# Optimization experiments

Hardware: AMD Instinct MI355X
Metric: run time of the kernel (lower is better)

The kernel has to match this reference:

```python
import jax, jax.numpy as jnp
import numpy as np

N = 500000      # gaussians
D = 256         # d_model
H = 8           # heads
DFF = 1024      # ffn hidden
L = 2           # encoder layers
VS = 0.0625     # voxel_size
MR = 10         # multires (both embedders)
EPS = 1e-5      # layernorm eps


def _embed(x, nf):
    freqs = 2.0 ** jnp.arange(nf, dtype=x.dtype)
    xf = x[..., None, :] * freqs[:, None]                  # [..., F, 3]
    sc = jnp.stack([jnp.sin(xf), jnp.cos(xf)], axis=-2)    # [..., F, 2, 3]
    return jnp.concatenate([x, sc.reshape(*x.shape[:-1], nf * 2 * 3)], axis=-1)


def _ln(x, w, b):
    m = x.mean(-1, keepdims=True)
    v = ((x - m) ** 2).mean(-1, keepdims=True)
    return (x - m) / jnp.sqrt(v + EPS) * w + b


def _mha(x, wi, bi, wo, bo):
    U, d = x.shape
    dh = d // H
    qkv = x @ wi.T + bi                                    # [U, 3d]
    q, k, v = jnp.split(qkv, 3, axis=-1)
    sp = lambda t: t.reshape(U, H, dh).transpose(1, 0, 2)  # [H, U, dh]
    q, k, v = sp(q), sp(k), sp(v)
    scale = 1.0 / jnp.sqrt(jnp.asarray(dh, x.dtype))
    attn = jax.nn.softmax(jnp.einsum('hqd,hkd->hqk', q, k) * scale, axis=-1)
    o = jnp.einsum('hqk,hkd->hqd', attn, v).transpose(1, 0, 2).reshape(U, d)
    return o @ wo.T + bo


def setup_inputs() -> dict:
    key = jax.random.key(0)
    ks = jax.random.split(key, 24)
    centres = jax.random.uniform(ks[0], (N, 3), dtype=jnp.float32)
    feats = jax.random.normal(ks[1], (N, D), dtype=jnp.float32)
    # voxelize + unique (data-dependent -> precompute, round() has zero grad anyway)
    vp = np.round(np.asarray(centres) / VS) * VS
    _, inv = np.unique(vp, axis=0, return_inverse=True)
    inv = inv.reshape(-1)
    U = int(inv.max()) + 1
    s = 0.02
    rn = lambda k, shp: jax.random.normal(k, shp, dtype=jnp.float32) * s
    PE = MR * 2 * 3 + 3  # 63
    return dict(
        gaussian_centres=centres,
        gaussian_features=feats,
        inverse_indices=jnp.asarray(inv, jnp.int32),
        num_unique=U,
        in_proj_w=rn(ks[2], (L, 3 * D, D)), in_proj_b=rn(ks[3], (L, 3 * D)),
        out_proj_w=rn(ks[4], (L, D, D)), out_proj_b=rn(ks[5], (L, D)),
        lin1_w=rn(ks[6], (L, DFF, D)), lin1_b=rn(ks[7], (L, DFF)),
        lin2_w=rn(ks[8], (L, D, DFF)), lin2_b=rn(ks[9], (L, D)),
        norm1_w=jnp.ones((L, D), jnp.float32), norm1_b=jnp.zeros((L, D), jnp.float32),
        norm2_w=jnp.ones((L, D), jnp.float32), norm2_b=jnp.zeros((L, D), jnp.float32),
        pe_w1=rn(ks[10], (D, PE)), pe_b1=rn(ks[11], (D,)),
        pe_w2=rn(ks[12], (D, D)), pe_b2=rn(ks[13], (D,)),
        dm_w1=rn(ks[14], (D, D + PE)), dm_b1=rn(ks[15], (D,)),
        dm_w2=rn(ks[16], (D, D)), dm_b2=rn(ks[17], (D,)),
    )


def reference(gaussian_centres, gaussian_features, inverse_indices, num_unique,
              in_proj_w, in_proj_b, out_proj_w, out_proj_b,
              lin1_w, lin1_b, lin2_w, lin2_b,
              norm1_w, norm1_b, norm2_w, norm2_b,
              pe_w1, pe_b1, pe_w2, pe_b2,
              dm_w1, dm_b1, dm_w2, dm_b2):
    # 1-4: voxelize + segment-sum features per unique voxel
    vp = jnp.round(gaussian_centres / VS) * VS
    agg = jax.ops.segment_sum(gaussian_features, inverse_indices, num_segments=num_unique)  # [U, D]
    uv = jnp.zeros((num_unique, 3), gaussian_centres.dtype).at[inverse_indices].set(vp)     # unique voxel coords
    # learnable positional encoding MLP
    pe = _embed(uv, MR)
    pe = jax.nn.leaky_relu(pe @ pe_w1.T + pe_b1, 0.01) @ pe_w2.T + pe_b2
    # transformer encoder (post-LN, relu, eval mode -> no dropout)
    x = agg + pe
    for l in range(L):
        x = _ln(x + _mha(x, in_proj_w[l], in_proj_b[l], out_proj_w[l], out_proj_b[l]),
                norm1_w[l], norm1_b[l])
        ff = jax.nn.relu(x @ lin1_w[l].T + lin1_b[l]) @ lin2_w[l].T + lin2_b[l]
        x = _ln(x + ff, norm2_w[l], norm2_b[l])
    # 6-7: gather back to per-gaussian rows
    rec = x[inverse_indices]                                # [N, D]
    # delta MLP: cat([pos_encoding, features])
    d_in = jnp.concatenate([_embed(gaussian_centres, MR), rec], axis=-1)
    delta = jax.nn.leaky_relu(d_in @ dm_w1.T + dm_b1, 0.01) @ dm_w2.T + dm_b2
    return rec + delta
```

## Files before the change

### kernel.cpp

```cpp
#include <hip/hip_runtime.h>
#include <math.h>

#define NG   500000
#define DM   256
#define NH   8
#define DHD  32
#define DFF  1024
#define NLAY 2
#define PED  63
#define VSF  0.0625f
#define EPSF 1e-5f
#define UP   4928
#define MAXU 4913
#define NQT  77
#define NDBLK 7813
#define SCL  0.17677669529663687f

typedef short bf16x8 __attribute__((ext_vector_type(8)));
typedef float f32x4 __attribute__((ext_vector_type(4)));

__device__ __forceinline__ float lrelu(float v){ return v >= 0.f ? v : 0.01f*v; }

__device__ __forceinline__ short f2b(float f){
  unsigned u = __float_as_uint(f);
  return (short)((u + 0x7fffu + ((u >> 16) & 1u)) >> 16);
}

__device__ __forceinline__ f32x4 mfma16(bf16x8 a, bf16x8 b, f32x4 c){
  return __builtin_amdgcn_mfma_f32_16x16x32_bf16(a, b, c, 0, 0, 0);
}

__device__ __forceinline__ float embed_elem(float cx, float cy, float cz, int j){
  if (j == 0) return cx;
  if (j == 1) return cy;
  if (j == 2) return cz;
  int q = j - 3;
  int f = q / 6;
  int r = q - f*6;
  int c = r % 3;
  float base = (c==0)?cx:((c==1)?cy:cz);
  float xf = base * (float)(1u << f);
  return (r < 3) ? sinf(xf) : cosf(xf);
}

__device__ __forceinline__ float wred(float v){
  #pragma unroll
  for (int o = 32; o > 0; o >>= 1) v += __shfl_xor(v, o);
  return v;
}

__global__ void zero_kernel(int* p, int n){
  int i = blockIdx.x*blockDim.x + threadIdx.x;
  if (i < n) p[i] = 0;
}

__global__ void prep_kernel(const float* __restrict__ centres, const int* __restrict__ inv,
                            int* __restrict__ counts, float* __restrict__ uv){
  for (int i = blockIdx.x*blockDim.x + threadIdx.x; i < NG; i += gridDim.x*blockDim.x){
    int v = inv[i];
    atomicAdd(&counts[v], 1);
    float vx = rintf(centres[i*3]   * 16.f) * VSF;
    float vy = rintf(centres[i*3+1] * 16.f) * VSF;
    float vz = rintf(centres[i*3+2] * 16.f) * VSF;
    uv[v*3] = vx; uv[v*3+1] = vy; uv[v*3+2] = vz;
  }
}

__global__ void scan_kernel(const int* __restrict__ counts, int* __restrict__ offs,
                            const int* __restrict__ pU){
  const int U = *pU;
  const int CH = 8;
  __shared__ int tot[1024];
  int tid = threadIdx.x;
  int base = tid * CH;
  int c[CH];
  int s = 0;
  #pragma unroll
  for (int i = 0; i < CH; ++i){
    int idx = base + i;
    int v = (idx < U) ? counts[idx] : 0;
    c[i] = s;
    s += v;
  }
  tot[tid] = s;
  __syncthreads();
  for (int o = 1; o < 1024; o <<= 1){
    int v = 0;
    if (tid >= o) v = tot[tid - o];
    __syncthreads();
    tot[tid] += v;
    __syncthreads();
  }
  int excl = tot[tid] - s;
  #pragma unroll
  for (int i = 0; i < CH; ++i){
    int idx = base + i;
    if (idx < U) offs[idx] = excl + c[i];
  }
}

__global__ void scatter_kernel(const int* __restrict__ inv, const int* __restrict__ offs,
                               int* __restrict__ cursor, int* __restrict__ gidx){
  for (int i = blockIdx.x*blockDim.x + threadIdx.x; i < NG; i += gridDim.x*blockDim.x){
    int v = inv[i];
    int p = atomicAdd(&cursor[v], 1);
    gidx[offs[v] + p] = i;
  }
}

__global__ void cvt_weights(const float* __restrict__ ipw, const float* __restrict__ opw,
                            const float* __restrict__ l1w, const float* __restrict__ l2w,
                            const float* __restrict__ dw1, const float* __restrict__ dw2,
                            short* ipwb, short* opwb, short* l1wb, short* l2wb,
                            short* dw2b, short* dw1bb, short* dw1ab){
  int i = blockIdx.x*256 + threadIdx.x;
  switch (blockIdx.y){
    case 0: if (i < 2*768*256)  ipwb[i] = f2b(ipw[i]); break;
    case 1: if (i < 2*256*256)  opwb[i] = f2b(opw[i]); break;
    case 2: if (i < 2*1024*256) l1wb[i] = f2b(l1w[i]); break;
    case 3: if (i < 2*256*1024) l2wb[i] = f2b(l2w[i]); break;
    case 4: if (i < 256*256)    dw2b[i] = f2b(dw2[i]); break;
    case 5: if (i < 256*256){ int r = i>>8, c = i&255; dw1bb[i] = f2b(dw1[r*319 + 63 + c]); } break;
    case 6: if (i < 256*64){  int r = i>>6, c = i&63;  dw1ab[i] = f2b(c < 63 ? dw1[r*319 + c] : 0.f); } break;
  }
}

__global__ __launch_bounds__(256) void agg_pe_kernel(const float* __restrict__ feats,
   const int* __restrict__ gidx, const int* __restrict__ offs, const int* __restrict__ counts,
   const float* __restrict__ uv, const float* __restrict__ pw1, const float* __restrict__ pb1,
   const float* __restrict__ pw2, const float* __restrict__ pb2,
   float* __restrict__ x, const int* __restrict__ pU){
  const int U = *pU;
  __shared__ int gl[512];
  __shared__ __align__(16) float4 red[256];
  __shared__ __align__(16) float e[PED];
  __shared__ __align__(16) float h[DM];
  const int t = threadIdx.x;
  const int c4 = t & 63;
  const int rr = t >> 6;
  for (int u = blockIdx.x; u < U; u += gridDim.x){
    const int o0 = offs[u], cnt = counts[u];
    float4 s = {0.f,0.f,0.f,0.f};
    for (int base = 0; base < cnt; base += 512){
      const int cc = min(cnt - base, 512);
      __syncthreads();
      for (int j = t; j < cc; j += 256) gl[j] = gidx[o0 + base + j];
      __syncthreads();
      int j = rr;
      for (; j + 8 <= cc; j += 8){
        const int r0 = gl[j], r1 = gl[j+4];
        float4 v0 = *reinterpret_cast<const float4*>(&feats[(size_t)r0*DM + c4*4]);
        float4 v1 = *reinterpret_cast<const float4*>(&feats[(size_t)r1*DM + c4*4]);
        s.x += v0.x + v1.x; s.y += v0.y + v1.y;
        s.z += v0.z + v1.z; s.w += v0.w + v1.w;
      }
      for (; j < cc; j += 4){
        float4 v0 = *reinterpret_cast<const float4*>(&feats[(size_t)gl[j]*DM + c4*4]);
        s.x += v0.x; s.y += v0.y; s.z += v0.z; s.w += v0.w;
      }
    }
    red[t] = s;
    if (t < PED)
      e[t] = embed_elem(uv[u*3], uv[u*3+1], uv[u*3+2], t);
    __syncthreads();
    if (rr == 0){
      float4 a = red[c4], b = red[64+c4], c = red[128+c4], d = red[192+c4];
      a.x += b.x + c.x + d.x; a.y += b.y + c.y + d.y;
      a.z += b.z + c.z + d.z; a.w += b.w + c.w + d.w;
      red[c4] = a;
    }
    __syncthreads();
    const float sum = reinterpret_cast<const float*>(red)[t];
    float a1 = pb1[t];
    const float* w1 = pw1 + t*PED;
    for (int k = 0; k < PED; ++k) a1 += w1[k]*e[k];
    h[t] = lrelu(a1);
    __syncthreads();
    float a2 = pb2[t];
    const float* w2 = pw2 + (size_t)t*DM;
    for (int k = 0; k < DM; k += 4){
      float4 w = *reinterpret_cast<const float4*>(w2+k);
      float4 hv = *reinterpret_cast<const float4*>(&h[k]);
      a2 += w.x*hv.x + w.y*hv.y + w.z*hv.z + w.w*hv.w;
    }
    x[(size_t)u*DM + t] = sum + a2;
    __syncthreads();
  }
}

template<int ACT, bool HASRES>
__global__ __launch_bounds__(256) void gemm_bf(const float* __restrict__ A,
    const short* __restrict__ Bbf, const float* __restrict__ bias,
    const float* __restrict__ res, float* __restrict__ C,
    const int K, const int Nn, const int* __restrict__ pU){
  const int M = *pU;
  const int r0 = blockIdx.x * 64;
  if (r0 >= M) return;
  const int n0 = blockIdx.y * 64;
  __shared__ __align__(16) short Al[64*32];
  const int tid = threadIdx.x;
  const int wid = tid >> 6, lane = tid & 63;
  const int l15 = lane & 15, l4 = lane >> 4;
  f32x4 acc[4];
  #pragma unroll
  for (int nt = 0; nt < 4; ++nt) acc[nt] = (f32x4){0.f,0.f,0.f,0.f};
  const int nk = K >> 5;
  const int srow = tid >> 2, se8 = (tid & 3) * 8;
  const int arowc = min(r0 + srow, M-1);
  for (int kc = 0; kc < nk; ++kc){
    {
      const float* ap = A + (size_t)arowc*K + kc*32 + se8;
      f32x4 a0 = *(const f32x4*)ap;
      f32x4 a1 = *(const f32x4*)(ap + 4);
      bf16x8 av;
      av[0]=f2b(a0[0]); av[1]=f2b(a0[1]); av[2]=f2b(a0[2]); av[3]=f2b(a0[3]);
      av[4]=f2b(a1[0]); av[5]=f2b(a1[1]); av[6]=f2b(a1[2]); av[7]=f2b(a1[3]);
      *(bf16x8*)&Al[(srow*32 + se8) ^ ((srow & 7) << 3)] = av;
    }
    __syncthreads();
    const int ar = 16*wid + l15;
    bf16x8 af = *(const bf16x8*)&Al[(ar*32 + 8*l4) ^ ((ar & 7) << 3)];
    #pragma unroll
    for (int nt = 0; nt < 4; ++nt){
      const short* bp = Bbf + (size_t)(n0 + 16*nt + l15)*K + kc*32 + 8*l4;
      bf16x8 bfr = *(const bf16x8*)bp;
      acc[nt] = mfma16(af, bfr, acc[nt]);
    }
    __syncthreads();
  }
  #pragma unroll
  for (int nt = 0; nt < 4; ++nt){
    const int col = n0 + 16*nt + l15;
    const float bv = bias[col];
    #pragma unroll
    for (int r = 0; r < 4; ++r){
      const int row = r0 + 16*wid + 4*l4 + r;
      if (row < M){
        float v = acc[nt][r] + bv;
        if (ACT == 1) v = fmaxf(v, 0.f);
        if (HASRES) v += res[(size_t)row*Nn + col];
        C[(size_t)row*Nn + col] = v;
      }
    }
  }
}

__global__ __launch_bounds__(256) void attn_mfma(const float* __restrict__ qkv,
                                                 float* __restrict__ y, const int* __restrict__ pU){
  const int U = *pU;
  const int bid = blockIdx.x;
  const int h = bid & 7, qt = bid >> 3;
  const int q0 = qt * 64;
  const int tid = threadIdx.x;
  const int wid = tid >> 6, lane = tid & 63;
  const int l15 = lane & 15, l4 = lane >> 4;
  __shared__ __align__(16) short Kl[64*32];
  __shared__ __align__(16) short Vt[32*64];
  __shared__ __align__(16) short Pl[4][64*16];

  const int qrow = min(q0 + 16*wid + l15, U-1);
  const float* qp = qkv + (size_t)qrow*768 + h*DHD + 8*l4;
  bf16x8 qf;
  {
    f32x4 q0v = *(const f32x4*)qp;
    f32x4 q1v = *(const f32x4*)(qp + 4);
    qf[0]=f2b(q0v[0]*SCL); qf[1]=f2b(q0v[1]*SCL); qf[2]=f2b(q0v[2]*SCL); qf[3]=f2b(q0v[3]*SCL);
    qf[4]=f2b(q1v[0]*SCL); qf[5]=f2b(q1v[1]*SCL); qf[6]=f2b(q1v[2]*SCL); qf[7]=f2b(q1v[3]*SCL);
  }
  f32x4 o0 = (f32x4){0.f,0.f,0.f,0.f}, o1 = (f32x4){0.f,0.f,0.f,0.f};
  float mrun = -INFINITY, lrun = 0.f;
  const int srow = tid >> 2, se8 = (tid & 3) * 8;
  const int ntile = (U + 63) >> 6;
  for (int kt = 0; kt < ntile; ++kt){
    const int kb = kt * 64;
    {
      const int krow = min(kb + srow, U-1);
      const float* kp = qkv + (size_t)krow*768 + DM + h*DHD + se8;
      f32x4 k0 = *(const f32x4*)kp;
      f32x4 k1 = *(const f32x4*)(kp + 4);
      bf16x8 kv;
      kv[0]=f2b(k0[0]); kv[1]=f2b(k0[1]); kv[2]=f2b(k0[2]); kv[3]=f2b(k0[3]);
      kv[4]=f2b(k1[0]); kv[5]=f2b(k1[1]); kv[6]=f2b(k1[2]); kv[7]=f2b(k1[3]);
      *(bf16x8*)&Kl[(srow*32 + se8) ^ ((srow & 7) << 3)] = kv;
      const float* vp = qkv + (size_t)krow*768 + 2*DM + h*DHD + se8;
      f32x4 v0 = *(const f32x4*)vp;
      f32x4 v1 = *(const f32x4*)(vp + 4);
      #pragma unroll
      for (int j = 0; j < 8; ++j){
        const int d = se8 + j;
        const float vv = (j < 4) ? v0[j & 3] : v1[j & 3];
        Vt[(d*64 + srow) ^ ((d & 7) << 3)] = f2b(vv);
      }
    }
    __syncthreads();
    float s[16];
    #pragma unroll
    for (int nt = 0; nt < 4; ++nt){
      const int row = 16*nt + l15;
      bf16x8 kf = *(const bf16x8*)&Kl[(row*32 + 8*l4) ^ ((row & 7) << 3)];
      f32x4 d = mfma16(kf, qf, (f32x4){0.f,0.f,0.f,0.f});
      const int kbase = kb + 16*nt + 4*l4;
      #pragma unroll
      for (int r = 0; r < 4; ++r)
        s[nt*4 + r] = (kbase + r < U) ? d[r] : -INFINITY;
    }
    float cm = s[0];
    #pragma unroll
    for (int i = 1; i < 16; ++i) cm = fmaxf(cm, s[i]);
    cm = fmaxf(cm, __shfl_xor(cm, 16));
    cm = fmaxf(cm, __shfl_xor(cm, 32));
    const float mnew = fmaxf(mrun, cm);
    const float f = __expf(mrun - mnew);
    float ls = 0.f;
    #pragma unroll
    for (int i = 0; i < 16; ++i){ s[i] = __expf(s[i] - mnew); ls += s[i]; }
    ls += __shfl_xor(ls, 16);
    ls += __shfl_xor(ls, 32);
    lrun = lrun * f + ls;
    o0 = o0 * f; o1 = o1 * f;
    mrun = mnew;
    #pragma unroll
    for (int nt = 0; nt < 4; ++nt)
      #pragma unroll
      for (int r = 0; r < 4; ++r){
        const int row = 16*nt + 4*l4 + r;
        Pl[wid][(row*16 + l15) ^ (((row >> 2) & 3) << 2)] = f2b(s[nt*4 + r]);
      }
    __syncthreads();
    #pragma unroll
    for (int kc = 0; kc < 2; ++kc){
      bf16x8 pf;
      #pragma unroll
      for (int j = 0; j < 8; ++j){
        const int row = 32*kc + 8*l4 + j;
        pf[j] = Pl[wid][(row*16 + l15) ^ (((row >> 2) & 3) << 2)];
      }
      {
        const int row = l15;
        bf16x8 vf = *(const bf16x8*)&Vt[(row*64 + 32*kc + 8*l4) ^ ((row & 7) << 3)];
        o0 = mfma16(vf, pf, o0);
      }
      {
        const int row = 16 + l15;
        bf16x8 vf = *(const bf16x8*)&Vt[(row*64 + 32*kc + 8*l4) ^ ((row & 7) << 3)];
        o1 = mfma16(vf, pf, o1);
      }
    }
    __syncthreads();
  }
  const float invl = 1.f / lrun;
  const int qg = q0 + 16*wid + l15;
  if (qg < U){
    float* yp = y + (size_t)qg*DM + h*DHD;
    #pragma unroll
    for (int r = 0; r < 4; ++r){
      yp[4*l4 + r]      = o0[r] * invl;
      yp[16 + 4*l4 + r] = o1[r] * invl;
    }
  }
}

__global__ __launch_bounds__(256) void ln_kernel(const float* __restrict__ in,
    const float* __restrict__ w, const float* __restrict__ b,
    float* __restrict__ out, const int* __restrict__ pU){
  const int U = *pU;
  const int t = threadIdx.x;
  const int wid = t >> 6;
  __shared__ float red[4];
  for (int u = blockIdx.x; u < U; u += gridDim.x){
    float v = in[(size_t)u*DM + t];
    float s = wred(v);
    if ((t & 63) == 0) red[wid] = s;
    __syncthreads();
    float mean = (red[0]+red[1]+red[2]+red[3]) * (1.f/DM);
    __syncthreads();
    float d = v - mean;
    float sq = wred(d*d);
    if ((t & 63) == 0) red[wid] = sq;
    __syncthreads();
    float var = (red[0]+red[1]+red[2]+red[3]) * (1.f/DM);
    out[(size_t)u*DM + t] = d * (1.0f/sqrtf(var + EPSF)) * w[t] + b[t];
    __syncthreads();
  }
}

__global__ __launch_bounds__(256) void delta_mfma(const float* __restrict__ centres,
   const int* __restrict__ inv, const int* __restrict__ gidx,
   const float* __restrict__ x, const float* __restrict__ rc,
   const short* __restrict__ w1abf, const short* __restrict__ w2bf,
   const float* __restrict__ db2, float* __restrict__ out){
  __shared__ __align__(16) float cs[64][3];
  __shared__ int ivl[64];
  __shared__ int sg[64];
  __shared__ __align__(16) short hl[64*256];
  const int tid = threadIdx.x;
  const int wid = tid >> 6, lane = tid & 63;
  const int l15 = lane & 15, l4 = lane >> 4;
  const int p0 = blockIdx.x * 64;
  if (tid < 64){
    const int pos = p0 + tid;
    const int gid = gidx[min(pos, NG-1)];
    sg[tid]  = (pos < NG) ? gid : -1;
    ivl[tid] = inv[gid];
    cs[tid][0] = centres[gid*3];
    cs[tid][1] = centres[gid*3+1];
    cs[tid][2] = centres[gid*3+2];
  }
  __syncthreads();
  const int arow = 16*wid + l15;
  const float cx = cs[arow][0], cy = cs[arow][1], cz = cs[arow][2];
  bf16x8 ef[2];
  #pragma unroll
  for (int kc = 0; kc < 2; ++kc)
    #pragma unroll
    for (int jj = 0; jj < 8; ++jj){
      const int j = kc*32 + 8*l4 + jj;
      ef[kc][jj] = f2b(j < PED ? embed_elem(cx, cy, cz, j) : 0.f);
    }
  const int glb = 16*wid + 4*l4;
  const int rv0 = ivl[glb], rv1 = ivl[glb+1], rv2 = ivl[glb+2], rv3 = ivl[glb+3];
  #pragma unroll
  for (int nt = 0; nt < 16; ++nt){
    const int c = 16*nt + l15;
    f32x4 a;
    a[0] = rc[(size_t)rv0*DM + c];
    a[1] = rc[(size_t)rv1*DM + c];
    a[2] = rc[(size_t)rv2*DM + c];
    a[3] = rc[(size_t)rv3*DM + c];
    #pragma unroll
    for (int kc = 0; kc < 2; ++kc){
      const bf16x8 bfr = *(const bf16x8*)&w1abf[(16*nt + l15)*64 + kc*32 + 8*l4];
      a = mfma16(ef[kc], bfr, a);
    }
    #pragma unroll
    for (int r = 0; r < 4; ++r){
      const int row = glb + r;
      hl[(row*256 + c) ^ ((row & 7) << 3)] = f2b(lrelu(a[r]));
    }
  }
  __syncthreads();
  bf16x8 hf[8];
  #pragma unroll
  for (int kc = 0; kc < 8; ++kc){
    const int row = 16*wid + l15;
    hf[kc] = *(const bf16x8*)&hl[(row*256 + kc*32 + 8*l4) ^ ((row & 7) << 3)];
  }
  const int g0 = sg[glb], g1 = sg[glb+1], g2 = sg[glb+2], g3 = sg[glb+3];
  #pragma unroll
  for (int half = 0; half < 2; ++half){
    f32x4 acc[8];
    #pragma unroll
    for (int q = 0; q < 8; ++q){
      const int c = half*128 + 16*q + l15;
      const float bv = db2[c];
      acc[q][0] = x[(size_t)rv0*DM + c] + bv;
      acc[q][1] = x[(size_t)rv1*DM + c] + bv;
      acc[q][2] = x[(size_t)rv2*DM + c] + bv;
      acc[q][3] = x[(size_t)rv3*DM + c] + bv;
    }
    #pragma unroll
    for (int kc = 0; kc < 8; ++kc)
      #pragma unroll
      for (int q = 0; q < 8; ++q){
        const int n = half*128 + 16*q + l15;
        const bf16x8 bfr = *(const bf16x8*)&w2bf[(size_t)n*256 + kc*32 + 8*l4];
        acc[q] = mfma16(hf[kc], bfr, acc[q]);
      }
    #pragma unroll
    for (int q = 0; q < 8; ++q){
      const int c = half*128 + 16*q + l15;
      if (g0 >= 0) out[(size_t)g0*DM + c] = acc[q][0];
      if (g1 >= 0) out[(size_t)g1*DM + c] = acc[q][1];
      if (g2 >= 0) out[(size_t)g2*DM + c] = acc[q][2];
      if (g3 >= 0) out[(size_t)g3*DM + c] = acc[q][3];
    }
  }
}

extern "C" void kernel_launch(void* const* d_in, const int* in_sizes, int n_in,
                              void* d_out, int out_size, void* d_ws, size_t ws_size,
                              hipStream_t stream){
  (void)in_sizes; (void)n_in; (void)out_size; (void)ws_size;
  const float* centres = (const float*)d_in[0];
  const float* feats   = (const float*)d_in[1];
  const int*   inv     = (const int*)d_in[2];
  const int*   pU      = (const int*)d_in[3];
  const float* ipw = (const float*)d_in[4];
  const float* ipb = (const float*)d_in[5];
  const float* opw = (const float*)d_in[6];
  const float* opb = (const float*)d_in[7];
  const float* l1w = (const float*)d_in[8];
  const float* l1b = (const float*)d_in[9];
  const float* l2w = (const float*)d_in[10];
  const float* l2b = (const float*)d_in[11];
  const float* n1w = (const float*)d_in[12];
  const float* n1b = (const float*)d_in[13];
  const float* n2w = (const float*)d_in[14];
  const float* n2b = (const float*)d_in[15];
  const float* pw1 = (const float*)d_in[16];
  const float* pb1 = (const float*)d_in[17];
  const float* pw2 = (const float*)d_in[18];
  const float* pb2 = (const float*)d_in[19];
  const float* dw1 = (const float*)d_in[20];
  const float* db1 = (const float*)d_in[21];
  const float* dw2 = (const float*)d_in[22];
  const float* db2 = (const float*)d_in[23];
  float* out = (float*)d_out;

  char* ws = (char*)d_ws;
  size_t off = 0;
  auto take = [&](size_t bytes)->char*{
    char* p = ws + off; off += (bytes + 255) & ~(size_t)255; return p;
  };
  float* xb   = (float*)take((size_t)UP*DM*4);
  float* yb   = (float*)take((size_t)UP*DM*4);
  float* big  = (float*)take((size_t)UP*DFF*4);
  float* rcb  = (float*)take((size_t)UP*DM*4);
  float* uv   = (float*)take((size_t)UP*3*4);
  int* counts = (int*)take((size_t)2*UP*4);
  int* cursor = counts + UP;
  int* offs   = (int*)take((size_t)UP*4);
  int* gidx   = (int*)take((size_t)NG*4);
  short* ipwbf  = (short*)take((size_t)2*768*256*2);
  short* opwbf  = (short*)take((size_t)2*256*256*2);
  short* l1wbf  = (short*)take((size_t)2*1024*256*2);
  short* l2wbf  = (short*)take((size_t)2*256*1024*2);
  short* dw2bf  = (short*)take((size_t)256*256*2);
  short* dw1bbf = (short*)take((size_t)256*256*2);
  short* dw1abf = (short*)take((size_t)256*64*2);

  zero_kernel<<<(2*UP + 255)/256, 256, 0, stream>>>(counts, 2*UP);
  prep_kernel<<<1024, 256, 0, stream>>>(centres, inv, counts, uv);
  scan_kernel<<<1, 1024, 0, stream>>>(counts, offs, pU);
  scatter_kernel<<<1024, 256, 0, stream>>>(inv, offs, cursor, gidx);
  cvt_weights<<<dim3(2048, 7), 256, 0, stream>>>(ipw, opw, l1w, l2w, dw1, dw2,
                                                 ipwbf, opwbf, l1wbf, l2wbf,
                                                 dw2bf, dw1bbf, dw1abf);
  agg_pe_kernel<<<MAXU, 256, 0, stream>>>(feats, gidx, offs, counts, uv,
                                          pw1, pb1, pw2, pb2, xb, pU);

  for (int l = 0; l < NLAY; ++l){
    gemm_bf<0,false><<<dim3(NQT,12), 256, 0, stream>>>(xb, ipwbf + (size_t)l*768*256,
        ipb + (size_t)l*768, nullptr, big, DM, 3*DM, pU);
    attn_mfma<<<8*NQT, 256, 0, stream>>>(big, yb, pU);
    gemm_bf<0,true><<<dim3(NQT,4), 256, 0, stream>>>(yb, opwbf + (size_t)l*256*256,
        opb + (size_t)l*DM, xb, big, DM, DM, pU);
    ln_kernel<<<1024, 256, 0, stream>>>(big, n1w + (size_t)l*DM, n1b + (size_t)l*DM, xb, pU);
    gemm_bf<1,false><<<dim3(NQT,16), 256, 0, stream>>>(xb, l1wbf + (size_t)l*1024*256,
        l1b + (size_t)l*DFF, nullptr, big, DM, DFF, pU);
    gemm_bf<0,true><<<dim3(NQT,4), 256, 0, stream>>>(big, l2wbf + (size_t)l*256*1024,
        l2b + (size_t)l*DM, xb, yb, DFF, DM, pU);
    ln_kernel<<<1024, 256, 0, stream>>>(yb, n2w + (size_t)l*DM, n2b + (size_t)l*DM, xb, pU);
  }

  gemm_bf<0,false><<<dim3(NQT,4), 256, 0, stream>>>(xb, dw1bbf, db1, nullptr, rcb, DM, DM, pU);
  delta_mfma<<<NDBLK, 256, 0, stream>>>(centres, inv, gidx, xb, rcb, dw1abf, dw2bf, db2, out);
}
```

Before: 2.473 ms.

## Process delta MLP per voxel and unroll segment-sum gather loop further

```diff
diff --git a/kernel.cpp b/kernel.cpp
--- a/kernel.cpp
+++ b/kernel.cpp
@@ -13,7 +13,6 @@
 #define UP   4928
 #define MAXU 4913
 #define NQT  77
-#define NDBLK 7813
 #define SCL  0.17677669529663687f
 
 typedef short bf16x8 __attribute__((ext_vector_type(8)));
@@ -147,12 +146,16 @@
       for (int j = t; j < cc; j += 256) gl[j] = gidx[o0 + base + j];
       __syncthreads();
       int j = rr;
-      for (; j + 8 <= cc; j += 8){
-        const int r0 = gl[j], r1 = gl[j+4];
+      for (; j + 16 <= cc; j += 16){
+        const int r0 = gl[j], r1 = gl[j+4], r2 = gl[j+8], r3 = gl[j+12];
         float4 v0 = *reinterpret_cast<const float4*>(&feats[(size_t)r0*DM + c4*4]);
         float4 v1 = *reinterpret_cast<const float4*>(&feats[(size_t)r1*DM + c4*4]);
-        s.x += v0.x + v1.x; s.y += v0.y + v1.y;
-        s.z += v0.z + v1.z; s.w += v0.w + v1.w;
+        float4 v2 = *reinterpret_cast<const float4*>(&feats[(size_t)r2*DM + c4*4]);
+        float4 v3 = *reinterpret_cast<const float4*>(&feats[(size_t)r3*DM + c4*4]);
+        s.x += (v0.x + v1.x) + (v2.x + v3.x);
+        s.y += (v0.y + v1.y) + (v2.y + v3.y);
+        s.z += (v0.z + v1.z) + (v2.z + v3.z);
+        s.w += (v0.w + v1.w) + (v2.w + v3.w);
       }
       for (; j < cc; j += 4){
         float4 v0 = *reinterpret_cast<const float4*>(&feats[(size_t)gl[j]*DM + c4*4]);
@@ -384,95 +387,103 @@
   }
 }
 
-__global__ __launch_bounds__(256) void delta_mfma(const float* __restrict__ centres,
-   const int* __restrict__ inv, const int* __restrict__ gidx,
+__global__ __launch_bounds__(256) void delta_voxel(const float* __restrict__ centres,
+   const int* __restrict__ gidx, const int* __restrict__ offs, const int* __restrict__ counts,
    const float* __restrict__ x, const float* __restrict__ rc,
    const short* __restrict__ w1abf, const short* __restrict__ w2bf,
-   const float* __restrict__ db2, float* __restrict__ out){
+   const float* __restrict__ db2, float* __restrict__ out, const int* __restrict__ pU){
+  const int U = *pU;
+  __shared__ __align__(16) float rrc[DM];
+  __shared__ __align__(16) float rx[DM];
   __shared__ __align__(16) float cs[64][3];
-  __shared__ int ivl[64];
   __shared__ int sg[64];
   __shared__ __align__(16) short hl[64*256];
   const int tid = threadIdx.x;
   const int wid = tid >> 6, lane = tid & 63;
   const int l15 = lane & 15, l4 = lane >> 4;
-  const int p0 = blockIdx.x * 64;
-  if (tid < 64){
-    const int pos = p0 + tid;
-    const int gid = gidx[min(pos, NG-1)];
-    sg[tid]  = (pos < NG) ? gid : -1;
-    ivl[tid] = inv[gid];
-    cs[tid][0] = centres[gid*3];
-    cs[tid][1] = centres[gid*3+1];
-    cs[tid][2] = centres[gid*3+2];
-  }
-  __syncthreads();
-  const int arow = 16*wid + l15;
-  const float cx = cs[arow][0], cy = cs[arow][1], cz = cs[arow][2];
-  bf16x8 ef[2];
-  #pragma unroll
-  for (int kc = 0; kc < 2; ++kc)
-    #pragma unroll
-    for (int jj = 0; jj < 8; ++jj){
-      const int j = kc*32 + 8*l4 + jj;
-      ef[kc][jj] = f2b(j < PED ? embed_elem(cx, cy, cz, j) : 0.f);
-    }
-  const int glb = 16*wid + 4*l4;
-  const int rv0 = ivl[glb], rv1 = ivl[glb+1], rv2 = ivl[glb+2], rv3 = ivl[glb+3];
-  #pragma unroll
-  for (int nt = 0; nt < 16; ++nt){
-    const int c = 16*nt + l15;
-    f32x4 a;
-    a[0] = rc[(size_t)rv0*DM + c];
-    a[1] = rc[(size_t)rv1*DM + c];
-    a[2] = rc[(size_t)rv2*DM + c];
-    a[3] = rc[(size_t)rv3*DM + c];
-    #pragma unroll
-    for (int kc = 0; kc < 2; ++kc){
-      const bf16x8 bfr = *(const bf16x8*)&w1abf[(16*nt + l15)*64 + kc*32 + 8*l4];
-      a = mfma16(ef[kc], bfr, a);
-    }
-    #pragma unroll
-    for (int r = 0; r < 4; ++r){
-      const int row = glb + r;
-      hl[(row*256 + c) ^ ((row & 7) << 3)] = f2b(lrelu(a[r]));
-    }
-  }
-  __syncthreads();
-  bf16x8 hf[8];
-  #pragma unroll
-  for (int kc = 0; kc < 8; ++kc){
-    const int row = 16*wid + l15;
-    hf[kc] = *(const bf16x8*)&hl[(row*256 + kc*32 + 8*l4) ^ ((row & 7) << 3)];
-  }
-  const int g0 = sg[glb], g1 = sg[glb+1], g2 = sg[glb+2], g3 = sg[glb+3];
-  #pragma unroll
-  for (int half = 0; half < 2; ++half){
-    f32x4 acc[8];
-    #pragma unroll
-    for (int q = 0; q < 8; ++q){
-      const int c = half*128 + 16*q + l15;
-      const float bv = db2[c];
-      acc[q][0] = x[(size_t)rv0*DM + c] + bv;
-      acc[q][1] = x[(size_t)rv1*DM + c] + bv;
-      acc[q][2] = x[(size_t)rv2*DM + c] + bv;
-      acc[q][3] = x[(size_t)rv3*DM + c] + bv;
-    }
-    #pragma unroll
-    for (int kc = 0; kc < 8; ++kc)
-      #pragma unroll
-      for (int q = 0; q < 8; ++q){
-        const int n = half*128 + 16*q + l15;
-        const bf16x8 bfr = *(const bf16x8*)&w2bf[(size_t)n*256 + kc*32 + 8*l4];
-        acc[q] = mfma16(hf[kc], bfr, acc[q]);
-      }
-    #pragma unroll
-    for (int q = 0; q < 8; ++q){
-      const int c = half*128 + 16*q + l15;
-      if (g0 >= 0) out[(size_t)g0*DM + c] = acc[q][0];
-      if (g1 >= 0) out[(size_t)g1*DM + c] = acc[q][1];
-      if (g2 >= 0) out[(size_t)g2*DM + c] = acc[q][2];
-      if (g3 >= 0) out[(size_t)g3*DM + c] = acc[q][3];
+  for (int u = blockIdx.x; u < U; u += gridDim.x){
+    __syncthreads();
+    rrc[tid] = rc[(size_t)u*DM + tid];
+    rx[tid]  = x[(size_t)u*DM + tid] + db2[tid];
+    __syncthreads();
+    float rcv[16], xv[16];
+    #pragma unroll
+    for (int nt = 0; nt < 16; ++nt){
+      rcv[nt] = rrc[16*nt + l15];
+      xv[nt]  = rx[16*nt + l15];
+    }
+    const int o0 = offs[u], cnt = counts[u];
+    for (int base = 0; base < cnt; base += 64){
+      __syncthreads();
+      if (tid < 64){
+        const int p = base + tid;
+        const int gid = (p < cnt) ? gidx[o0 + p] : -1;
+        sg[tid] = gid;
+        const int cg = (gid >= 0) ? gid : gidx[o0];
+        cs[tid][0] = centres[cg*3];
+        cs[tid][1] = centres[cg*3+1];
+        cs[tid][2] = centres[cg*3+2];
+      }
+      __syncthreads();
+      const int arow = 16*wid + l15;
+      const float cx = cs[arow][0], cy = cs[arow][1], cz = cs[arow][2];
+      bf16x8 ef[2];
+      #pragma unroll
+      for (int kc = 0; kc < 2; ++kc)
+        #pragma unroll
+        for (int jj = 0; jj < 8; ++jj){
+          const int j = kc*32 + 8*l4 + jj;
+          ef[kc][jj] = f2b(j < PED ? embed_elem(cx, cy, cz, j) : 0.f);
+        }
+      const int glb = 16*wid + 4*l4;
+      #pragma unroll
+      for (int nt = 0; nt < 16; ++nt){
+        const int c = 16*nt + l15;
+        f32x4 a = (f32x4){rcv[nt], rcv[nt], rcv[nt], rcv[nt]};
+        #pragma unroll
+        for (int kc = 0; kc < 2; ++kc){
+          const bf16x8 bfr = *(const bf16x8*)&w1abf[(16*nt + l15)*64 + kc*32 + 8*l4];
+          a = mfma16(ef[kc], bfr, a);
+        }
+        #pragma unroll
+        for (int r = 0; r < 4; ++r){
+          const int row = glb + r;
+          hl[(row*256 + c) ^ ((row & 7) << 3)] = f2b(lrelu(a[r]));
+        }
+      }
+      __syncthreads();
+      bf16x8 hf[8];
+      #pragma unroll
+      for (int kc = 0; kc < 8; ++kc){
+        const int row = 16*wid + l15;
+        hf[kc] = *(const bf16x8*)&hl[(row*256 + kc*32 + 8*l4) ^ ((row & 7) << 3)];
+      }
+      const int g0 = sg[glb], g1 = sg[glb+1], g2 = sg[glb+2], g3 = sg[glb+3];
+      #pragma unroll
+      for (int half = 0; half < 2; ++half){
+        f32x4 acc[8];
+        #pragma unroll
+        for (int q = 0; q < 8; ++q){
+          const float xb = xv[half*8 + q];
+          acc[q] = (f32x4){xb, xb, xb, xb};
+        }
+        #pragma unroll
+        for (int kc = 0; kc < 8; ++kc)
+          #pragma unroll
+          for (int q = 0; q < 8; ++q){
+            const int n = half*128 + 16*q + l15;
+            const bf16x8 bfr = *(const bf16x8*)&w2bf[(size_t)n*256 + kc*32 + 8*l4];
+            acc[q] = mfma16(hf[kc], bfr, acc[q]);
+          }
+        #pragma unroll
+        for (int q = 0; q < 8; ++q){
+          const int c = half*128 + 16*q + l15;
+          if (g0 >= 0) out[(size_t)g0*DM + c] = acc[q][0];
+          if (g1 >= 0) out[(size_t)g1*DM + c] = acc[q][1];
+          if (g2 >= 0) out[(size_t)g2*DM + c] = acc[q][2];
+          if (g3 >= 0) out[(size_t)g3*DM + c] = acc[q][3];
+        }
+      }
     }
   }
 }
@@ -554,5 +565,6 @@
   }
 
   gemm_bf<0,false><<<dim3(NQT,4), 256, 0, stream>>>(xb, dw1bbf, db1, nullptr, rcb, DM, DM, pU);
-  delta_mfma<<<NDBLK, 256, 0, stream>>>(centres, inv, gidx, xb, rcb, dw1abf, dw2bf, db2, out);
-}
+  delta_voxel<<<MAXU, 256, 0, stream>>>(centres, gidx, offs, counts, xb, rcb,
+                                        dw1abf, dw2bf, db2, out, pU);
+}
```

Measured after the change: 5.442 ms. 120% more time.
